# Kernel optimization log

Hardware: AMD Instinct MI355X
Metric: run time of the kernel (lower is better)

The kernel has to match this reference:

```python
import jax, jax.numpy as jnp
import numpy as np

K = 64        # top-k from init_kwargs
TAU = 1.0     # temperature at step=0: tau_start*(1-0) + tau_end*0


def setup_inputs() -> dict:
    key = jax.random.key(0)
    k1, k2 = jax.random.split(key)
    B, N = 2048, 8192
    logits = jax.random.normal(k1, (B, N), dtype=jnp.float32)
    # gumbels = -log(Exp(1)) == standard Gumbel noise
    gumbel_noise = jax.random.gumbel(k2, (B, N), dtype=jnp.float32)
    return {"logits": logits, "gumbel_noise": gumbel_noise}


def reference(logits, gumbel_noise):
    # training path of GumbelTopK (step=0 -> tau=TAU, hard=True)
    g = (logits + gumbel_noise) / TAU                       # [B, N]
    order = jnp.argsort(-g, axis=-1)                        # descending sort order
    sorted_g = jnp.take_along_axis(g, order, axis=-1)
    cumsum = jnp.cumsum(jax.nn.softmax(sorted_g, axis=-1), axis=-1)
    mask = (cumsum <= K).astype(sorted_g.dtype)             # NB: faithful to source (<= k)
    sorted_y = mask * jax.nn.softmax(sorted_g / TAU, axis=-1)
    # scatter back to original positions == gather by inverse permutation
    inv = jnp.argsort(order, axis=-1)
    y = jnp.take_along_axis(sorted_y, inv, axis=-1)         # [B, N]
    # hard straight-through: one-hot-k of y
    k = min(K, y.shape[-1])
    _, idx = jax.lax.top_k(y, k)                            # [B, k]
    rows = jnp.arange(y.shape[0])[:, None]
    y_hard = jnp.zeros_like(y).at[rows, idx].set(1.0)
    return jax.lax.stop_gradient(y_hard - y) + y
```

## Files before the change

### kernel.cpp

```cpp
#include <hip/hip_runtime.h>

constexpr int N = 8192;
constexpr int K = 64;
constexpr int THREADS = 256;
constexpr int WAVES = THREADS / 64;
constexpr int EPT = N / THREADS;
constexpr int VEC = EPT / 4;
constexpr int CAP = 3072;

__device__ __forceinline__ unsigned orderable(float f) {
    unsigned x = __float_as_uint(f);
    return (x & 0x80000000u) ? ~x : (x | 0x80000000u);
}

__global__ __launch_bounds__(THREADS, 4)
void gumbel_topk_onehot(const float* __restrict__ logits,
                        const float* __restrict__ noise,
                        float* __restrict__ out)
{
    __shared__ unsigned hist[2048];
    __shared__ unsigned cand[CAP];
    __shared__ unsigned wavesum[WAVES];
    __shared__ unsigned ccount;
    __shared__ unsigned sel_bin, sel_kth, sel_cnt;

    const int tid  = threadIdx.x;
    const int lane = tid & 63;
    const int wave = tid >> 6;
    const long long row = blockIdx.x;

    const float4* lrow = (const float4*)(logits + row * (long long)N);
    const float4* nrow = (const float4*)(noise  + row * (long long)N);

    unsigned key[EPT];
#pragma unroll
    for (int i = 0; i < VEC; ++i) {
        int idx = tid + i * THREADS;
        float4 a = lrow[idx];
        float4 b = nrow[idx];
        key[4*i+0] = orderable(a.x + b.x);
        key[4*i+1] = orderable(a.y + b.y);
        key[4*i+2] = orderable(a.z + b.z);
        key[4*i+3] = orderable(a.w + b.w);
    }

    {
        uint4 z = make_uint4(0,0,0,0);
        for (int i = tid; i < 512; i += THREADS) ((uint4*)hist)[i] = z;
    }
    if (tid == 0) ccount = 0;
    __syncthreads();
#pragma unroll
    for (int e = 0; e < EPT; ++e)
        atomicAdd(&hist[key[e] >> 21], 1u);
    __syncthreads();

    unsigned kth = K;

#define SELECT_BIN(BPT)                                                      \
    {                                                                        \
        unsigned p = 0;                                                      \
        _Pragma("unroll")                                                    \
        for (int j = 0; j < (BPT); ++j) p += hist[tid * (BPT) + j];          \
        unsigned s = p;                                                      \
        _Pragma("unroll")                                                    \
        for (int off = 1; off < 64; off <<= 1) {                             \
            unsigned v = __shfl_down(s, off);                                \
            if (lane + off < 64) s += v;                                     \
        }                                                                    \
        if (lane == 0) wavesum[wave] = s;                                    \
        __syncthreads();                                                     \
        unsigned S = s;                                                      \
        _Pragma("unroll")                                                    \
        for (int w = 0; w < WAVES; ++w) if (w > wave) S += wavesum[w];       \
        unsigned Snext = S - p;                                              \
        if (S >= kth && Snext < kth) {                                       \
            unsigned cum = Snext;                                            \
            for (int j = (BPT) - 1; j >= 0; --j) {                           \
                unsigned c = hist[tid * (BPT) + j];                          \
                if (cum + c >= kth) {                                        \
                    sel_bin = (unsigned)(tid * (BPT) + j);                   \
                    sel_kth = kth - cum;                                     \
                    sel_cnt = c;                                             \
                    break;                                                   \
                }                                                            \
                cum += c;                                                    \
            }                                                                \
        }                                                                    \
        __syncthreads();                                                     \
    }

    SELECT_BIN(8)
    const unsigned b1   = sel_bin;
    const unsigned cnt1 = sel_cnt;
    kth = sel_kth;
    __syncthreads();

    const bool use_cand = (cnt1 <= (unsigned)CAP);
#pragma unroll
    for (int e = 0; e < EPT; ++e) {
        if ((key[e] >> 21) == b1) {
            unsigned pos = atomicAdd(&ccount, 1u);
            if (pos < (unsigned)CAP) cand[pos] = key[e] & 0x1FFFFFu;
        }
    }

    __syncthreads();
    {
        uint4 z = make_uint4(0,0,0,0);
        for (int i = tid; i < 512; i += THREADS) ((uint4*)hist)[i] = z;
    }
    __syncthreads();
    if (use_cand) {
        for (int i = tid; i < (int)cnt1; i += THREADS)
            atomicAdd(&hist[cand[i] >> 10], 1u);
    } else {
#pragma unroll
        for (int e = 0; e < EPT; ++e)
            if ((key[e] >> 21) == b1)
                atomicAdd(&hist[(key[e] >> 10) & 0x7FFu], 1u);
    }
    __syncthreads();

    SELECT_BIN(8)
    const unsigned b2 = sel_bin;
    kth = sel_kth;
    __syncthreads();

    {
        uint4 z = make_uint4(0,0,0,0);
        for (int i = tid; i < 256; i += THREADS) ((uint4*)hist)[i] = z;
    }
    __syncthreads();
    if (use_cand) {
        for (int i = tid; i < (int)cnt1; i += THREADS) {
            unsigned cv = cand[i];
            if ((cv >> 10) == b2) atomicAdd(&hist[cv & 0x3FFu], 1u);
        }
    } else {
        const unsigned pfx = (b1 << 11) | b2;
#pragma unroll
        for (int e = 0; e < EPT; ++e)
            if ((key[e] >> 10) == pfx)
                atomicAdd(&hist[key[e] & 0x3FFu], 1u);
    }
    __syncthreads();

    SELECT_BIN(4)
    const unsigned b3      = sel_bin;
    const unsigned take_eq = sel_kth;
    const unsigned c_eq    = sel_cnt;

    const unsigned T = (b1 << 21) | (b2 << 10) | b3;
    const bool fast = (take_eq == c_eq);

    float4* orow = (float4*)(out + row * (long long)N);
#pragma unroll
    for (int i = 0; i < VEC; ++i) {
        int idx = tid + i * THREADS;
        float4 o;
        o.x = (key[4*i+0] > T || (fast && key[4*i+0] == T)) ? 1.0f : 0.0f;
        o.y = (key[4*i+1] > T || (fast && key[4*i+1] == T)) ? 1.0f : 0.0f;
        o.z = (key[4*i+2] > T || (fast && key[4*i+2] == T)) ? 1.0f : 0.0f;
        o.w = (key[4*i+3] > T || (fast && key[4*i+3] == T)) ? 1.0f : 0.0f;
        orow[idx] = o;
    }

    if (!fast) {
        __syncthreads();
        if (tid == 0) {
            const float* lf = logits + row * (long long)N;
            const float* nf = noise  + row * (long long)N;
            float* of = out + row * (long long)N;
            unsigned c = 0;
            for (int i = 0; i < N; ++i) {
                if (orderable(lf[i] + nf[i]) == T) {
                    of[i] = 1.0f;
                    if (++c == take_eq) break;
                }
            }
        }
    }
#undef SELECT_BIN
}

extern "C" void kernel_launch(void* const* d_in, const int* in_sizes, int n_in,
                              void* d_out, int out_size, void* d_ws, size_t ws_size,
                              hipStream_t stream) {
    const float* logits = (const float*)d_in[0];
    const float* noise  = (const float*)d_in[1];
    float* out = (float*)d_out;
    const int rows = in_sizes[0] / N;
    gumbel_topk_onehot<<<rows, THREADS, 0, stream>>>(logits, noise, out);
}
```

Baseline: 172.1 us.

## Replace later radix passes with rank-by-comparison selection for small candidate sets

Doubles the block to 512 threads, with 16 keys per thread and a higher occupancy hint. When the first-level bin holds at most 512 candidates, each thread ranks its candidate by comparing it against all the others, which finds the exact threshold and replaces the second and third histogram passes and their barriers. The change also zeroes the histogram before the loads, drops one barrier, and writes the output with nontemporal stores. The quadratic comparison loop costs more when the candidate count is large, and the larger block changes register pressure.

```diff
diff --git a/kernel.cpp b/kernel.cpp
--- a/kernel.cpp
+++ b/kernel.cpp
@@ -2,27 +2,30 @@
 
 constexpr int N = 8192;
 constexpr int K = 64;
-constexpr int THREADS = 256;
+constexpr int THREADS = 512;
 constexpr int WAVES = THREADS / 64;
 constexpr int EPT = N / THREADS;
 constexpr int VEC = EPT / 4;
 constexpr int CAP = 3072;
 
+typedef float f32x4 __attribute__((ext_vector_type(4)));
+
 __device__ __forceinline__ unsigned orderable(float f) {
     unsigned x = __float_as_uint(f);
     return (x & 0x80000000u) ? ~x : (x | 0x80000000u);
 }
 
-__global__ __launch_bounds__(THREADS, 4)
+__global__ __launch_bounds__(THREADS, 8)
 void gumbel_topk_onehot(const float* __restrict__ logits,
                         const float* __restrict__ noise,
                         float* __restrict__ out)
 {
-    __shared__ unsigned hist[2048];
-    __shared__ unsigned cand[CAP];
+    __shared__ __align__(16) unsigned hist[2048];
+    __shared__ __align__(16) unsigned cand[CAP];
     __shared__ unsigned wavesum[WAVES];
     __shared__ unsigned ccount;
     __shared__ unsigned sel_bin, sel_kth, sel_cnt;
+    __shared__ unsigned r_val, r_take, r_ceq;
 
     const int tid  = threadIdx.x;
     const int lane = tid & 63;
@@ -31,6 +34,9 @@
 
     const float4* lrow = (const float4*)(logits + row * (long long)N);
     const float4* nrow = (const float4*)(noise  + row * (long long)N);
+
+    ((uint4*)hist)[tid] = make_uint4(0, 0, 0, 0);
+    if (tid == 0) ccount = 0;
 
     unsigned key[EPT];
 #pragma unroll
@@ -43,13 +49,8 @@
         key[4*i+2] = orderable(a.z + b.z);
         key[4*i+3] = orderable(a.w + b.w);
     }
-
-    {
-        uint4 z = make_uint4(0,0,0,0);
-        for (int i = tid; i < 512; i += THREADS) ((uint4*)hist)[i] = z;
-    }
-    if (tid == 0) ccount = 0;
     __syncthreads();
+
 #pragma unroll
     for (int e = 0; e < EPT; ++e)
         atomicAdd(&hist[key[e] >> 21], 1u);
@@ -90,13 +91,11 @@
         __syncthreads();                                                     \
     }
 
-    SELECT_BIN(8)
+    SELECT_BIN(4)
     const unsigned b1   = sel_bin;
     const unsigned cnt1 = sel_cnt;
     kth = sel_kth;
-    __syncthreads();
-
-    const bool use_cand = (cnt1 <= (unsigned)CAP);
+
 #pragma unroll
     for (int e = 0; e < EPT; ++e) {
         if ((key[e] >> 21) == b1) {
@@ -104,66 +103,84 @@
             if (pos < (unsigned)CAP) cand[pos] = key[e] & 0x1FFFFFu;
         }
     }
-
     __syncthreads();
-    {
-        uint4 z = make_uint4(0,0,0,0);
-        for (int i = tid; i < 512; i += THREADS) ((uint4*)hist)[i] = z;
-    }
-    __syncthreads();
-    if (use_cand) {
-        for (int i = tid; i < (int)cnt1; i += THREADS)
-            atomicAdd(&hist[cand[i] >> 10], 1u);
+
+    unsigned T, take_eq, c_eq;
+
+    if (cnt1 <= (unsigned)THREADS) {
+        const bool have = (tid < (int)cnt1);
+        const unsigned myv = have ? cand[tid] : 0u;
+        unsigned g = 0, eq = 0;
+#pragma unroll 4
+        for (int j = 0; j < (int)cnt1; ++j) {
+            unsigned v = cand[j];
+            g  += (v >  myv) ? 1u : 0u;
+            eq += (v == myv) ? 1u : 0u;
+        }
+        if (have && g < kth && g + eq >= kth) {
+            r_val  = myv;
+            r_take = kth - g;
+            r_ceq  = eq;
+        }
+        __syncthreads();
+        T       = (b1 << 21) | r_val;
+        take_eq = r_take;
+        c_eq    = r_ceq;
     } else {
-#pragma unroll
-        for (int e = 0; e < EPT; ++e)
-            if ((key[e] >> 21) == b1)
-                atomicAdd(&hist[(key[e] >> 10) & 0x7FFu], 1u);
-    }
-    __syncthreads();
-
-    SELECT_BIN(8)
-    const unsigned b2 = sel_bin;
-    kth = sel_kth;
-    __syncthreads();
-
-    {
-        uint4 z = make_uint4(0,0,0,0);
-        for (int i = tid; i < 256; i += THREADS) ((uint4*)hist)[i] = z;
-    }
-    __syncthreads();
-    if (use_cand) {
-        for (int i = tid; i < (int)cnt1; i += THREADS) {
-            unsigned cv = cand[i];
-            if ((cv >> 10) == b2) atomicAdd(&hist[cv & 0x3FFu], 1u);
-        }
-    } else {
-        const unsigned pfx = (b1 << 11) | b2;
-#pragma unroll
-        for (int e = 0; e < EPT; ++e)
-            if ((key[e] >> 10) == pfx)
-                atomicAdd(&hist[key[e] & 0x3FFu], 1u);
-    }
-    __syncthreads();
-
-    SELECT_BIN(4)
-    const unsigned b3      = sel_bin;
-    const unsigned take_eq = sel_kth;
-    const unsigned c_eq    = sel_cnt;
-
-    const unsigned T = (b1 << 21) | (b2 << 10) | b3;
+        const bool use_cand = (cnt1 <= (unsigned)CAP);
+
+        ((uint4*)hist)[tid] = make_uint4(0, 0, 0, 0);
+        __syncthreads();
+        if (use_cand) {
+            for (int i = tid; i < (int)cnt1; i += THREADS)
+                atomicAdd(&hist[cand[i] >> 10], 1u);
+        } else {
+#pragma unroll
+            for (int e = 0; e < EPT; ++e)
+                if ((key[e] >> 21) == b1)
+                    atomicAdd(&hist[(key[e] >> 10) & 0x7FFu], 1u);
+        }
+        __syncthreads();
+
+        SELECT_BIN(4)
+        const unsigned b2 = sel_bin;
+        kth = sel_kth;
+        __syncthreads();
+
+        if (tid < 256) ((uint4*)hist)[tid] = make_uint4(0, 0, 0, 0);
+        __syncthreads();
+        if (use_cand) {
+            for (int i = tid; i < (int)cnt1; i += THREADS) {
+                unsigned cv = cand[i];
+                if ((cv >> 10) == b2) atomicAdd(&hist[cv & 0x3FFu], 1u);
+            }
+        } else {
+            const unsigned pfx = (b1 << 11) | b2;
+#pragma unroll
+            for (int e = 0; e < EPT; ++e)
+                if ((key[e] >> 10) == pfx)
+                    atomicAdd(&hist[key[e] & 0x3FFu], 1u);
+        }
+        __syncthreads();
+
+        SELECT_BIN(2)
+        T       = (b1 << 21) | (b2 << 10) | sel_bin;
+        take_eq = sel_kth;
+        c_eq    = sel_cnt;
+    }
+
     const bool fast = (take_eq == c_eq);
 
-    float4* orow = (float4*)(out + row * (long long)N);
+    f32x4* orow = (f32x4*)(out + row * (long long)N);
 #pragma unroll
     for (int i = 0; i < VEC; ++i) {
         int idx = tid + i * THREADS;
-        float4 o;
+        f32x4 o;
         o.x = (key[4*i+0] > T || (fast && key[4*i+0] == T)) ? 1.0f : 0.0f;
         o.y = (key[4*i+1] > T || (fast && key[4*i+1] == T)) ? 1.0f : 0.0f;
         o.z = (key[4*i+2] > T || (fast && key[4*i+2] == T)) ? 1.0f : 0.0f;
         o.w = (key[4*i+3] > T || (fast && key[4*i+3] == T)) ? 1.0f : 0.0f;
-        orow[idx] = o;
+        __builtin_nontemporal_store(o, &orow[idx]);
     }
 
     if (!fast) {
```

Result: no change. 174.2 us (+1.3%).

## Use one wave per row with fixed-threshold candidate filter and rank select

Applied to the files above, without the earlier changes.

Each wave now handles one row. A single streaming pass writes zeros with nontemporal stores and uses ballots to collect elements above a fixed value threshold into a small per-wave LDS buffer. The top-64 are then chosen by pairwise rank counting over those candidates. If the candidate count falls outside [K, 256], it falls back to a four-round 8-bit radix select that re-reads the row from global memory. This removes block-wide syncs and large-histogram atomics, but depends on the threshold suiting the input distribution and makes the fallback path expensive.

```diff
diff --git a/kernel.cpp b/kernel.cpp
--- a/kernel.cpp
+++ b/kernel.cpp
@@ -3,185 +3,205 @@
 constexpr int N = 8192;
 constexpr int K = 64;
 constexpr int THREADS = 256;
-constexpr int WAVES = THREADS / 64;
-constexpr int EPT = N / THREADS;
-constexpr int VEC = EPT / 4;
-constexpr int CAP = 3072;
+constexpr int WPB = THREADS / 64;
+constexpr int CHUNKS = N / 256;
+constexpr int WCAP = 256;
+
+constexpr float FTHRESH = 4.75f;
+
+typedef float f32x4 __attribute__((ext_vector_type(4)));
 
 __device__ __forceinline__ unsigned orderable(float f) {
     unsigned x = __float_as_uint(f);
     return (x & 0x80000000u) ? ~x : (x | 0x80000000u);
 }
 
-__global__ __launch_bounds__(THREADS, 4)
+__global__ __launch_bounds__(THREADS, 2)
 void gumbel_topk_onehot(const float* __restrict__ logits,
                         const float* __restrict__ noise,
                         float* __restrict__ out)
 {
-    __shared__ unsigned hist[2048];
-    __shared__ unsigned cand[CAP];
-    __shared__ unsigned wavesum[WAVES];
-    __shared__ unsigned ccount;
-    __shared__ unsigned sel_bin, sel_kth, sel_cnt;
-
-    const int tid  = threadIdx.x;
-    const int lane = tid & 63;
-    const int wave = tid >> 6;
-    const long long row = blockIdx.x;
-
-    const float4* lrow = (const float4*)(logits + row * (long long)N);
-    const float4* nrow = (const float4*)(noise  + row * (long long)N);
-
-    unsigned key[EPT];
+    __shared__ float    cval[WPB][WCAP];
+    __shared__ unsigned cidx[WPB][WCAP];
+
+    const int lane = threadIdx.x & 63;
+    const int w    = threadIdx.x >> 6;
+    const long long row = (long long)blockIdx.x * WPB + w;
+
+    const f32x4* l4 = (const f32x4*)(logits + row * (long long)N);
+    const f32x4* n4 = (const f32x4*)(noise  + row * (long long)N);
+    f32x4*       o4 = (f32x4*)(out + row * (long long)N);
+    float*     orow = out + row * (long long)N;
+
+    float*    mv = cval[w];
+    unsigned* mi = cidx[w];
+    const unsigned long long below = (1ull << lane) - 1ull;
+
+    unsigned c = 0;
+    f32x4 zero4 = {0.f, 0.f, 0.f, 0.f};
+#pragma unroll 8
+    for (int ch = 0; ch < CHUNKS; ++ch) {
+        f32x4 a = l4[ch * 64 + lane];
+        f32x4 b = n4[ch * 64 + lane];
+        f32x4 s = a + b;
+        __builtin_nontemporal_store(zero4, &o4[ch * 64 + lane]);
+        const unsigned ebase = (unsigned)(ch * 256 + lane * 4);
 #pragma unroll
-    for (int i = 0; i < VEC; ++i) {
-        int idx = tid + i * THREADS;
-        float4 a = lrow[idx];
-        float4 b = nrow[idx];
-        key[4*i+0] = orderable(a.x + b.x);
-        key[4*i+1] = orderable(a.y + b.y);
-        key[4*i+2] = orderable(a.z + b.z);
-        key[4*i+3] = orderable(a.w + b.w);
+        for (int e = 0; e < 4; ++e) {
+            const bool p = (s[e] >= FTHRESH);
+            unsigned long long m = __ballot(p);
+            if (p) {
+                unsigned pos = c + (unsigned)__popcll(m & below);
+                if (pos < (unsigned)WCAP) { mv[pos] = s[e]; mi[pos] = ebase + e; }
+            }
+            c += (unsigned)__popcll(m);
+        }
     }
-
-    {
-        uint4 z = make_uint4(0,0,0,0);
-        for (int i = tid; i < 512; i += THREADS) ((uint4*)hist)[i] = z;
+    asm volatile("s_waitcnt lgkmcnt(0)" ::: "memory");
+
+    if (c >= (unsigned)K && c <= (unsigned)WCAP) {
+        const unsigned j1 = lane + 64, j2 = lane + 128, j3 = lane + 192;
+        const float v0 = ((unsigned)lane < c) ? mv[lane] : 0.f;
+        const float v1 = (j1 < c) ? mv[j1] : 0.f;
+        const float v2 = (j2 < c) ? mv[j2] : 0.f;
+        const float v3 = (j3 < c) ? mv[j3] : 0.f;
+        unsigned g0=0,g1=0,g2=0,g3=0,e0=0,e1=0,e2=0,e3=0;
+        for (unsigned j = 0; j < c; ++j) {
+            const float vj = mv[j];
+            g0 += vj > v0; e0 += vj == v0;
+            g1 += vj > v1; e1 += vj == v1;
+            g2 += vj > v2; e2 += vj == v2;
+            g3 += vj > v3; e3 += vj == v3;
+        }
+        const bool f0 = ((unsigned)lane < c) && g0 < (unsigned)K && g0 + e0 >= (unsigned)K;
+        const bool f1 = (j1 < c) && g1 < (unsigned)K && g1 + e1 >= (unsigned)K;
+        const bool f2 = (j2 < c) && g2 < (unsigned)K && g2 + e2 >= (unsigned)K;
+        const bool f3 = (j3 < c) && g3 < (unsigned)K && g3 + e3 >= (unsigned)K;
+        float t = 0.f; unsigned tk = 0, ce = 0;
+        if (f0) { t = v0; tk = (unsigned)K - g0; ce = e0; }
+        if (f1) { t = v1; tk = (unsigned)K - g1; ce = e1; }
+        if (f2) { t = v2; tk = (unsigned)K - g2; ce = e2; }
+        if (f3) { t = v3; tk = (unsigned)K - g3; ce = e3; }
+        const unsigned long long fm = __ballot(f0 | f1 | f2 | f3);
+        const int src = __ffsll((long long)fm) - 1;
+        const float Tf = __shfl(t, src);
+        const unsigned take_eq = (unsigned)__shfl((int)tk, src);
+        const unsigned c_eq    = (unsigned)__shfl((int)ce, src);
+        const bool fast = (take_eq == c_eq);
+
+        asm volatile("s_waitcnt vmcnt(0)" ::: "memory");
+        if ((unsigned)lane < c && (v0 > Tf || (fast && v0 == Tf))) orow[mi[lane]] = 1.0f;
+        if (j1 < c && (v1 > Tf || (fast && v1 == Tf))) orow[mi[j1]] = 1.0f;
+        if (j2 < c && (v2 > Tf || (fast && v2 == Tf))) orow[mi[j2]] = 1.0f;
+        if (j3 < c && (v3 > Tf || (fast && v3 == Tf))) orow[mi[j3]] = 1.0f;
+
+        if (!fast) {
+            const unsigned i0 = ((unsigned)lane < c) ? mi[lane] : 0u;
+            const unsigned i1 = (j1 < c) ? mi[j1] : 0u;
+            const unsigned i2 = (j2 < c) ? mi[j2] : 0u;
+            const unsigned i3 = (j3 < c) ? mi[j3] : 0u;
+            unsigned r0=0,r1=0,r2=0,r3=0;
+            for (unsigned j = 0; j < c; ++j) {
+                const bool q = (mv[j] == Tf);
+                const unsigned ij = mi[j];
+                r0 += q && (ij < i0); r1 += q && (ij < i1);
+                r2 += q && (ij < i2); r3 += q && (ij < i3);
+            }
+            if ((unsigned)lane < c && v0 == Tf && r0 < take_eq) orow[i0] = 1.0f;
+            if (j1 < c && v1 == Tf && r1 < take_eq) orow[i1] = 1.0f;
+            if (j2 < c && v2 == Tf && r2 < take_eq) orow[i2] = 1.0f;
+            if (j3 < c && v3 == Tf && r3 < take_eq) orow[i3] = 1.0f;
+        }
+    } else {
+        unsigned* wh = (unsigned*)mv;
+        unsigned prefix = 0, kth = (unsigned)K, ceq = 0;
+#pragma unroll 1
+        for (int rnd = 0; rnd < 4; ++rnd) {
+            const int shift = 24 - 8 * rnd;
+            wh[lane] = 0; wh[lane+64] = 0; wh[lane+128] = 0; wh[lane+192] = 0;
+            asm volatile("s_waitcnt lgkmcnt(0)" ::: "memory");
+            for (int ch = 0; ch < CHUNKS; ++ch) {
+                f32x4 a = l4[ch * 64 + lane];
+                f32x4 b = n4[ch * 64 + lane];
+#pragma unroll
+                for (int e = 0; e < 4; ++e) {
+                    const unsigned key = orderable(a[e] + b[e]);
+                    const bool in = (rnd == 0) || ((key >> (unsigned)(shift + 8)) == prefix);
+                    if (in) atomicAdd(&wh[(key >> shift) & 255u], 1u);
+                }
+            }
+            asm volatile("s_waitcnt lgkmcnt(0)" ::: "memory");
+            const unsigned h0 = wh[4*lane+0], h1 = wh[4*lane+1];
+            const unsigned h2 = wh[4*lane+2], h3 = wh[4*lane+3];
+            const unsigned p = h0 + h1 + h2 + h3;
+            unsigned S = p;
+#pragma unroll
+            for (int off = 1; off < 64; off <<= 1) {
+                const unsigned v = __shfl_down(S, off);
+                if (lane + off < 64) S += v;
+            }
+            const unsigned Snext = S - p;
+            const bool win = (S >= kth) && (Snext < kth);
+            unsigned bin = 0, nk = 0, bc = 0;
+            if (win) {
+                unsigned cum = Snext;
+                if (cum + h3 >= kth)      { bin = 4u*lane+3; nk = kth - cum; bc = h3; }
+                else { cum += h3;
+                if (cum + h2 >= kth)      { bin = 4u*lane+2; nk = kth - cum; bc = h2; }
+                else { cum += h2;
+                if (cum + h1 >= kth)      { bin = 4u*lane+1; nk = kth - cum; bc = h1; }
+                else { cum += h1;
+                                            bin = 4u*lane+0; nk = kth - cum; bc = h0; } } }
+            }
+            const unsigned long long wm = __ballot(win);
+            const int src = __ffsll((long long)wm) - 1;
+            bin = (unsigned)__shfl((int)bin, src);
+            kth = (unsigned)__shfl((int)nk, src);
+            ceq = (unsigned)__shfl((int)bc, src);
+            prefix = (prefix << 8) | bin;
+        }
+        const unsigned Tord = prefix;
+        const unsigned take_eq = kth;
+        const bool fast = (take_eq == ceq);
+
+        asm volatile("s_waitcnt vmcnt(0)" ::: "memory");
+        unsigned rem = take_eq;
+        for (int ch = 0; ch < CHUNKS; ++ch) {
+            f32x4 a = l4[ch * 64 + lane];
+            f32x4 b = n4[ch * 64 + lane];
+            const unsigned k0 = orderable(a[0] + b[0]);
+            const unsigned k1 = orderable(a[1] + b[1]);
+            const unsigned k2 = orderable(a[2] + b[2]);
+            const unsigned k3 = orderable(a[3] + b[3]);
+            const unsigned ebase = (unsigned)(ch * 256 + lane * 4);
+            if (fast) {
+                if (k0 >= Tord) orow[ebase+0] = 1.0f;
+                if (k1 >= Tord) orow[ebase+1] = 1.0f;
+                if (k2 >= Tord) orow[ebase+2] = 1.0f;
+                if (k3 >= Tord) orow[ebase+3] = 1.0f;
+            } else {
+                if (k0 > Tord) orow[ebase+0] = 1.0f;
+                if (k1 > Tord) orow[ebase+1] = 1.0f;
+                if (k2 > Tord) orow[ebase+2] = 1.0f;
+                if (k3 > Tord) orow[ebase+3] = 1.0f;
+                const unsigned long long b0 = __ballot(k0 == Tord);
+                const unsigned long long b1 = __ballot(k1 == Tord);
+                const unsigned long long b2 = __ballot(k2 == Tord);
+                const unsigned long long b3 = __ballot(k3 == Tord);
+                if (rem) {
+                    unsigned r = (unsigned)(__popcll(b0 & below) + __popcll(b1 & below)
+                                          + __popcll(b2 & below) + __popcll(b3 & below));
+                    if (k0 == Tord) { if (r < rem) orow[ebase+0] = 1.0f; ++r; }
+                    if (k1 == Tord) { if (r < rem) orow[ebase+1] = 1.0f; ++r; }
+                    if (k2 == Tord) { if (r < rem) orow[ebase+2] = 1.0f; ++r; }
+                    if (k3 == Tord) { if (r < rem) orow[ebase+3] = 1.0f; ++r; }
+                }
+                const unsigned tot = (unsigned)(__popcll(b0) + __popcll(b1)
+                                              + __popcll(b2) + __popcll(b3));
+                rem = (rem > tot) ? rem - tot : 0u;
+            }
+        }
     }
-    if (tid == 0) ccount = 0;
-    __syncthreads();
-#pragma unroll
-    for (int e = 0; e < EPT; ++e)
-        atomicAdd(&hist[key[e] >> 21], 1u);
-    __syncthreads();
-
-    unsigned kth = K;
-
-#define SELECT_BIN(BPT)                                                      \
-    {                                                                        \
-        unsigned p = 0;                                                      \
-        _Pragma("unroll")                                                    \
-        for (int j = 0; j < (BPT); ++j) p += hist[tid * (BPT) + j];          \
-        unsigned s = p;                                                      \
-        _Pragma("unroll")                                                    \
-        for (int off = 1; off < 64; off <<= 1) {                             \
-            unsigned v = __shfl_down(s, off);                                \
-            if (lane + off < 64) s += v;                                     \
-        }                                                                    \
-        if (lane == 0) wavesum[wave] = s;                                    \
-        __syncthreads();                                                     \
-        unsigned S = s;                                                      \
-        _Pragma("unroll")                                                    \
-        for (int w = 0; w < WAVES; ++w) if (w > wave) S += wavesum[w];       \
-        unsigned Snext = S - p;                                              \
-        if (S >= kth && Snext < kth) {                                       \
-            unsigned cum = Snext;                                            \
-            for (int j = (BPT) - 1; j >= 0; --j) {                           \
-                unsigned c = hist[tid * (BPT) + j];                          \
-                if (cum + c >= kth) {                                        \
-                    sel_bin = (unsigned)(tid * (BPT) + j);                   \
-                    sel_kth = kth - cum;                                     \
-                    sel_cnt = c;                                             \
-                    break;                                                   \
-                }                                                            \
-                cum += c;                                                    \
-            }                                                                \
-        }                                                                    \
-        __syncthreads();                                                     \
-    }
-
-    SELECT_BIN(8)
-    const unsigned b1   = sel_bin;
-    const unsigned cnt1 = sel_cnt;
-    kth = sel_kth;
-    __syncthreads();
-
-    const bool use_cand = (cnt1 <= (unsigned)CAP);
-#pragma unroll
-    for (int e = 0; e < EPT; ++e) {
-        if ((key[e] >> 21) == b1) {
-            unsigned pos = atomicAdd(&ccount, 1u);
-            if (pos < (unsigned)CAP) cand[pos] = key[e] & 0x1FFFFFu;
-        }
-    }
-
-    __syncthreads();
-    {
-        uint4 z = make_uint4(0,0,0,0);
-        for (int i = tid; i < 512; i += THREADS) ((uint4*)hist)[i] = z;
-    }
-    __syncthreads();
-    if (use_cand) {
-        for (int i = tid; i < (int)cnt1; i += THREADS)
-            atomicAdd(&hist[cand[i] >> 10], 1u);
-    } else {
-#pragma unroll
-        for (int e = 0; e < EPT; ++e)
-            if ((key[e] >> 21) == b1)
-                atomicAdd(&hist[(key[e] >> 10) & 0x7FFu], 1u);
-    }
-    __syncthreads();
-
-    SELECT_BIN(8)
-    const unsigned b2 = sel_bin;
-    kth = sel_kth;
-    __syncthreads();
-
-    {
-        uint4 z = make_uint4(0,0,0,0);
-        for (int i = tid; i < 256; i += THREADS) ((uint4*)hist)[i] = z;
-    }
-    __syncthreads();
-    if (use_cand) {
-        for (int i = tid; i < (int)cnt1; i += THREADS) {
-            unsigned cv = cand[i];
-            if ((cv >> 10) == b2) atomicAdd(&hist[cv & 0x3FFu], 1u);
-        }
-    } else {
-        const unsigned pfx = (b1 << 11) | b2;
-#pragma unroll
-        for (int e = 0; e < EPT; ++e)
-            if ((key[e] >> 10) == pfx)
-                atomicAdd(&hist[key[e] & 0x3FFu], 1u);
-    }
-    __syncthreads();
-
-    SELECT_BIN(4)
-    const unsigned b3      = sel_bin;
-    const unsigned take_eq = sel_kth;
-    const unsigned c_eq    = sel_cnt;
-
-    const unsigned T = (b1 << 21) | (b2 << 10) | b3;
-    const bool fast = (take_eq == c_eq);
-
-    float4* orow = (float4*)(out + row * (long long)N);
-#pragma unroll
-    for (int i = 0; i < VEC; ++i) {
-        int idx = tid + i * THREADS;
-        float4 o;
-        o.x = (key[4*i+0] > T || (fast && key[4*i+0] == T)) ? 1.0f : 0.0f;
-        o.y = (key[4*i+1] > T || (fast && key[4*i+1] == T)) ? 1.0f : 0.0f;
-        o.z = (key[4*i+2] > T || (fast && key[4*i+2] == T)) ? 1.0f : 0.0f;
-        o.w = (key[4*i+3] > T || (fast && key[4*i+3] == T)) ? 1.0f : 0.0f;
-        orow[idx] = o;
-    }
-
-    if (!fast) {
-        __syncthreads();
-        if (tid == 0) {
-            const float* lf = logits + row * (long long)N;
-            const float* nf = noise  + row * (long long)N;
-            float* of = out + row * (long long)N;
-            unsigned c = 0;
-            for (int i = 0; i < N; ++i) {
-                if (orderable(lf[i] + nf[i]) == T) {
-                    of[i] = 1.0f;
-                    if (++c == take_eq) break;
-                }
-            }
-        }
-    }
-#undef SELECT_BIN
 }
 
 extern "C" void kernel_launch(void* const* d_in, const int* in_sizes, int n_in,
@@ -191,5 +211,5 @@
     const float* noise  = (const float*)d_in[1];
     float* out = (float*)d_out;
     const int rows = in_sizes[0] / N;
-    gumbel_topk_onehot<<<rows, THREADS, 0, stream>>>(logits, noise, out);
+    gumbel_topk_onehot<<<rows / WPB, THREADS, 0, stream>>>(logits, noise, out);
 }
```

After: 184.4 us. 1.07x slower.
